# Optimization experiments

Hardware: AMD Instinct MI355X
Metric: run time of the kernel (lower is better)

## Reference

```python
import jax, jax.numpy as jnp
import numpy as np

N, E, H, C, G = 100000, 400000, 4, 64, 64  # nodes, edges, heads, per-head dim, graphs
NEG_SLOPE = 0.2


def gat_conv(x, src, dst, W, a_src, a_dst, b, num_nodes):
    # PyG GATConv (v1), concat=True, eval mode (no dropout).
    h = (x @ W).reshape(num_nodes, H, C)                      # [N,H,C]
    al_src = (h * a_src).sum(-1)                              # [N,H]
    al_dst = (h * a_dst).sum(-1)                              # [N,H]
    e = jax.nn.leaky_relu(al_src[src] + al_dst[dst], NEG_SLOPE)  # [E',H]
    # segment softmax over incoming edges of each destination node
    m = jax.ops.segment_max(e, dst, num_segments=num_nodes)
    m = jnp.where(jnp.isfinite(m), m, 0.0)
    ex = jnp.exp(e - m[dst])
    s = jax.ops.segment_sum(ex, dst, num_segments=num_nodes)
    alpha = ex / (s[dst] + 1e-16)                             # [E',H]
    msg = h[src] * alpha[..., None]                           # [E',H,C]
    out = jax.ops.segment_sum(msg, dst, num_segments=num_nodes)
    return out.reshape(num_nodes, H * C) + b


def setup_inputs() -> dict:
    key = jax.random.key(0)
    ks = jax.random.split(key, 20)
    p = lambda k, shape: (jax.random.normal(k, shape, dtype=jnp.float32) * 0.05)
    inp = {
        "x": jax.random.normal(ks[0], (N, 2), dtype=jnp.float32),
        "edge_index": jax.random.randint(ks[1], (2, E), 0, N, dtype=jnp.int64),
        "batch": jnp.sort(jax.random.randint(ks[2], (N,), 0, G, dtype=jnp.int64)),
        # layer 1: in=2 -> heads*hidden=256
        "W1": p(ks[3], (2, H * C)), "a1s": p(ks[4], (H, C)), "a1d": p(ks[5], (H, C)), "b1": jnp.zeros((H * C,), jnp.float32),
        # layer 2,3: 256 -> 256
        "W2": p(ks[6], (H * C, H * C)), "a2s": p(ks[7], (H, C)), "a2d": p(ks[8], (H, C)), "b2": jnp.zeros((H * C,), jnp.float32),
        "W3": p(ks[9], (H * C, H * C)), "a3s": p(ks[10], (H, C)), "a3d": p(ks[11], (H, C)), "b3": jnp.zeros((H * C,), jnp.float32),
        # projection MLP 256 -> 512 -> 256
        "Wp1": p(ks[12], (H * C, 512)), "bp1": jnp.zeros((512,), jnp.float32),
        "Wp2": p(ks[13], (512, 256)), "bp2": jnp.zeros((256,), jnp.float32),
    }
    return inp


def reference(x, edge_index, batch, W1, a1s, a1d, b1, W2, a2s, a2d, b2,
              W3, a3s, a3d, b3, Wp1, bp1, Wp2, bp2):
    num_nodes = x.shape[0]
    # add_self_loops=True (PyG GATConv default); same edge set for all layers
    loops = jnp.arange(num_nodes, dtype=edge_index.dtype)
    src = jnp.concatenate([edge_index[0], loops])
    dst = jnp.concatenate([edge_index[1], loops])

    h = jax.nn.elu(gat_conv(x, src, dst, W1, a1s, a1d, b1, num_nodes))
    h = jax.nn.elu(gat_conv(h, src, dst, W2, a2s, a2d, b2, num_nodes))
    h = jax.nn.elu(gat_conv(h, src, dst, W3, a3s, a3d, b3, num_nodes))

    # global_mean_pool over graphs
    sums = jax.ops.segment_sum(h, batch, num_segments=G)            # [G,256]
    cnts = jax.ops.segment_sum(jnp.ones((num_nodes,), h.dtype), batch, num_segments=G)
    pooled = sums / jnp.maximum(cnts, 1.0)[:, None]

    # projection MLP (dropout is identity in eval)
    z = jax.nn.relu(pooled @ Wp1 + bp1)
    return z @ Wp2 + bp2
```

## Files before the change

### kernel.cpp

```cpp
#include <hip/hip_runtime.h>
#include <math.h>

#define HC 256
#define NHEAD 4
#define NEG_SLOPE 0.2f
#define GG 64

typedef unsigned short u16;
typedef unsigned int u32;
typedef __attribute__((ext_vector_type(8))) short short8;
typedef __attribute__((ext_vector_type(4))) float f32x4;

static __device__ inline u16 f2bf_rn(float f) {
  u32 x = __float_as_uint(f);
  u32 r = (x + 0x7fffu + ((x >> 16) & 1u)) >> 16;
  return (u16)r;
}
static __device__ inline float bf2f(u16 u) { return __uint_as_float(((u32)u) << 16); }


__global__ void count_deg_kernel(const int* __restrict__ ei, int E, int Nn, int* __restrict__ deg) {
  int idx = blockIdx.x * 256 + threadIdx.x;
  int Et = E + Nn;
  if (idx >= Et) return;
  int d = (idx < E) ? ei[E + idx] : (idx - E);
  atomicAdd(&deg[d], 1);
}

__global__ void scan_partial_kernel(const int* __restrict__ deg, int Nn,
                                    int* __restrict__ rowptr, int* __restrict__ bsum) {
  __shared__ int s[256];
  int t = threadIdx.x, i = blockIdx.x * 256 + t;
  int v = (i < Nn) ? deg[i] : 0;
  s[t] = v; __syncthreads();
  for (int off = 1; off < 256; off <<= 1) {
    int x = (t >= off) ? s[t - off] : 0; __syncthreads();
    s[t] += x; __syncthreads();
  }
  if (i < Nn) rowptr[i] = s[t] - v;
  if (t == 255) bsum[blockIdx.x] = s[t];
}

__global__ void scan_bsum_kernel(int* __restrict__ bsum, int nb) {
  __shared__ int s[512];
  int t = threadIdx.x;
  int v = (t < nb) ? bsum[t] : 0;
  s[t] = v; __syncthreads();
  for (int off = 1; off < 512; off <<= 1) {
    int x = (t >= off) ? s[t - off] : 0; __syncthreads();
    s[t] += x; __syncthreads();
  }
  if (t < nb) bsum[t] = s[t] - v;
}

__global__ void scan_add_kernel(int* __restrict__ rowptr, const int* __restrict__ bsum,
                                int Nn, int Etot) {
  int i = blockIdx.x * 256 + threadIdx.x;
  if (i < Nn) rowptr[i] += bsum[blockIdx.x];
  if (i == 0) rowptr[Nn] = Etot;
}

__global__ void fill_csr_kernel(const int* __restrict__ ei, int E, int Nn,
                                const int* __restrict__ rowptr, int* __restrict__ cursor,
                                int* __restrict__ col) {
  int idx = blockIdx.x * 256 + threadIdx.x;
  int Et = E + Nn;
  if (idx >= Et) return;
  int s, d;
  if (idx < E) { s = ei[idx]; d = ei[E + idx]; } else { s = d = idx - E; }
  int pos = atomicAdd(&cursor[d], 1);
  col[rowptr[d] + pos] = s;
}


__global__ void prep_misc_kernel(const float* __restrict__ W2, const float* __restrict__ W3,
                                 u16* __restrict__ W2t, u16* __restrict__ W3t,
                                 const int* __restrict__ batch, int Nn, int* __restrict__ bounds) {
  int b = blockIdx.x;
  if (b < 512) {
    const float* W = (b < 256) ? W2 : W3;
    u16* dst = (b < 256) ? W2t : W3t;
    int idx = (b & 255) * 256 + threadIdx.x;
    int k = idx >> 8, n = idx & 255;
    dst[n * 256 + k] = f2bf_rn(W[idx]);
  } else {
    int g = threadIdx.x;
    if (g > GG) return;
    int lo = 0, hi = Nn;
    while (lo < hi) { int mid = (lo + hi) >> 1; if (batch[mid] < g) lo = mid + 1; else hi = mid; }
    bounds[g] = lo;
  }
}


__global__ __launch_bounds__(256) void l1_fused_kernel(const float* __restrict__ x,
    const float* __restrict__ W1, const float* __restrict__ a1s, const float* __restrict__ a1d,
    const int* __restrict__ rowptr, const int* __restrict__ col,
    float* __restrict__ xbar, int Nn) {
  __shared__ float va[16];
  int t = threadIdx.x, q = t >> 6, lane = t & 63;
  {
    float asv = a1s[t], adv = a1d[t];
    float w0 = W1[t], w1 = W1[256 + t];
    float s0 = w0 * asv, s1 = w1 * asv, d0 = w0 * adv, d1 = w1 * adv;
    #pragma unroll
    for (int off = 32; off >= 1; off >>= 1) {
      s0 += __shfl_xor(s0, off, 64); s1 += __shfl_xor(s1, off, 64);
      d0 += __shfl_xor(d0, off, 64); d1 += __shfl_xor(d1, off, 64);
    }
    if (lane == 0) { va[q] = s0; va[4 + q] = s1; va[8 + q] = d0; va[12 + q] = d1; }
  }
  __syncthreads();
  int node = blockIdx.x * 256 + t;
  if (node >= Nn) return;
  float4 vs0 = *(const float4*)&va[0], vs1 = *(const float4*)&va[4];
  float4 vd0 = *(const float4*)&va[8], vd1 = *(const float4*)&va[12];
  float2 xv = *(const float2*)&x[(size_t)node * 2];
  float ad0 = xv.x * vd0.x + xv.y * vd1.x;
  float ad1 = xv.x * vd0.y + xv.y * vd1.y;
  float ad2 = xv.x * vd0.z + xv.y * vd1.z;
  float ad3 = xv.x * vd0.w + xv.y * vd1.w;
  int rs = rowptr[node], re = rowptr[node + 1];
  float S0 = 0.f, S1 = 0.f, S2 = 0.f, S3 = 0.f;
  float a0 = 0.f, a1 = 0.f, a2 = 0.f, a3 = 0.f, a4 = 0.f, a5 = 0.f, a6 = 0.f, a7 = 0.f;
  for (int i = rs; i < re; ++i) {
    int s = col[i];
    float2 xs = *(const float2*)&x[(size_t)s * 2];
    float e0 = xs.x * vs0.x + xs.y * vs1.x + ad0; e0 = e0 > 0.f ? e0 : NEG_SLOPE * e0;
    float e1 = xs.x * vs0.y + xs.y * vs1.y + ad1; e1 = e1 > 0.f ? e1 : NEG_SLOPE * e1;
    float e2 = xs.x * vs0.z + xs.y * vs1.z + ad2; e2 = e2 > 0.f ? e2 : NEG_SLOPE * e2;
    float e3 = xs.x * vs0.w + xs.y * vs1.w + ad3; e3 = e3 > 0.f ? e3 : NEG_SLOPE * e3;
    float p0 = __expf(e0), p1 = __expf(e1), p2 = __expf(e2), p3 = __expf(e3);
    S0 += p0; S1 += p1; S2 += p2; S3 += p3;
    a0 += p0 * xs.x; a1 += p0 * xs.y;
    a2 += p1 * xs.x; a3 += p1 * xs.y;
    a4 += p2 * xs.x; a5 += p2 * xs.y;
    a6 += p3 * xs.x; a7 += p3 * xs.y;
  }
  float i0 = 1.f / (S0 + 1e-16f), i1 = 1.f / (S1 + 1e-16f);
  float i2 = 1.f / (S2 + 1e-16f), i3 = 1.f / (S3 + 1e-16f);
  *(float4*)&xbar[(size_t)node * 8]     = make_float4(a0 * i0, a1 * i0, a2 * i1, a3 * i1);
  *(float4*)&xbar[(size_t)node * 8 + 4] = make_float4(a4 * i2, a5 * i2, a6 * i3, a7 * i3);
}

__global__ __launch_bounds__(256) void expand1_kernel(const float* __restrict__ xbar,
    const float* __restrict__ W1, const float* __restrict__ b1,
    u16* __restrict__ out16, int Nn) {
  int node = blockIdx.x * 4 + (threadIdx.x >> 6);
  int lane = threadIdx.x & 63;
  if (node >= Nn) return;
  int hA = lane >> 5;
  float4 xb0 = *(const float4*)&xbar[(size_t)node * 8];
  float4 xb1 = *(const float4*)&xbar[(size_t)node * 8 + 4];
  float xA0 = hA ? xb0.z : xb0.x, xA1 = hA ? xb0.w : xb0.y;
  float xB0 = hA ? xb1.z : xb1.x, xB1 = hA ? xb1.w : xb1.y;
  int cA = 2 * lane, cB = 128 + 2 * lane;
  float2 wA0 = *(const float2*)&W1[cA], wA1 = *(const float2*)&W1[256 + cA];
  float2 wB0 = *(const float2*)&W1[cB], wB1 = *(const float2*)&W1[256 + cB];
  float2 bA = *(const float2*)&b1[cA],  bB = *(const float2*)&b1[cB];
  float o0 = xA0 * wA0.x + xA1 * wA1.x + bA.x;
  float o1 = xA0 * wA0.y + xA1 * wA1.y + bA.y;
  float o2 = xB0 * wB0.x + xB1 * wB1.x + bB.x;
  float o3 = xB0 * wB0.y + xB1 * wB1.y + bB.y;
  o0 = o0 > 0.f ? o0 : (__expf(o0) - 1.0f);
  o1 = o1 > 0.f ? o1 : (__expf(o1) - 1.0f);
  o2 = o2 > 0.f ? o2 : (__expf(o2) - 1.0f);
  o3 = o3 > 0.f ? o3 : (__expf(o3) - 1.0f);
  u32* o32 = (u32*)out16;
  o32[(size_t)node * 128 + lane]      = (u32)f2bf_rn(o0) | ((u32)f2bf_rn(o1) << 16);
  o32[(size_t)node * 128 + 64 + lane] = (u32)f2bf_rn(o2) | ((u32)f2bf_rn(o3) << 16);
}


#define GBM 64
#define GBN 128

__global__ __launch_bounds__(256) void gemm_mfma_kernel(
    const u16* __restrict__ A, const u16* __restrict__ Bt,
    const float* __restrict__ as_, const float* __restrict__ ad_,
    u16* __restrict__ C16, float* __restrict__ als, float* __restrict__ ald, int Mrows) {
  __shared__ __align__(16) u16 smem[24576];
  char* base_ = (char*)smem;
  int bc = blockIdx.x, br = blockIdx.y;
  int tid = threadIdx.x;
  int wid = tid >> 6, lane = tid & 63;
  int wr = wid >> 1, wc = wid & 1;
  int row0 = br * GBM, col0 = bc * GBN;
  int fr = lane & 15, fg = lane >> 4;

  const u16* agp[2];
  int wofA[2];
  #pragma unroll
  for (int p = 0; p < 2; ++p) {
    int row = p * 32 + (tid >> 3), c = tid & 7;
    int gr = row0 + row; if (gr >= Mrows) gr = Mrows - 1;
    agp[p] = A + (size_t)gr * 256 + c * 8;
    wofA[p] = row * 128 + ((c ^ (row & 7)) << 4);
  }
  const u16* bgp[4];
  int wofB[4];
  #pragma unroll
  for (int p = 0; p < 4; ++p) {
    int row = p * 32 + (tid >> 3), c = tid & 7;
    bgp[p] = Bt + (size_t)(col0 + row) * 256 + c * 8;
    wofB[p] = row * 128 + ((c ^ (row & 7)) << 4);
  }
  int rofA[2][2], rofB[2][4];
  #pragma unroll
  for (int ks = 0; ks < 2; ++ks) {
    #pragma unroll
    for (int m = 0; m < 2; ++m) {
      int rl = wr * 32 + m * 16 + fr;
      rofA[ks][m] = rl * 128 + (((ks * 4 + fg) ^ (rl & 7)) << 4);
    }
    #pragma unroll
    for (int n = 0; n < 4; ++n) {
      int cl_ = wc * 64 + n * 16 + fr;
      rofB[ks][n] = cl_ * 128 + (((ks * 4 + fg) ^ (cl_ & 7)) << 4);
    }
  }

  f32x4 acc[2][4];
  #pragma unroll
  for (int m = 0; m < 2; ++m)
    #pragma unroll
    for (int n = 0; n < 4; ++n) acc[m][n] = (f32x4){0.f, 0.f, 0.f, 0.f};

  uint4 va[2], vb[4];
  #pragma unroll
  for (int p = 0; p < 2; ++p) va[p] = *(const uint4*)agp[p];
  #pragma unroll
  for (int p = 0; p < 4; ++p) vb[p] = *(const uint4*)bgp[p];
  #pragma unroll
  for (int p = 0; p < 2; ++p) *(uint4*)(base_ + wofA[p]) = va[p];
  #pragma unroll
  for (int p = 0; p < 4; ++p) *(uint4*)(base_ + 16384 + wofB[p]) = vb[p];
  __syncthreads();

  #pragma unroll
  for (int kt = 0; kt < 4; ++kt) {
    int buf = kt & 1;
    if (kt < 3) {
      #pragma unroll
      for (int p = 0; p < 2; ++p) va[p] = *(const uint4*)(agp[p] + (kt + 1) * 64);
      #pragma unroll
      for (int p = 0; p < 4; ++p) vb[p] = *(const uint4*)(bgp[p] + (kt + 1) * 64);
    }
    #pragma unroll
    for (int ks = 0; ks < 2; ++ks) {
      short8 af[2], bf[4];
      #pragma unroll
      for (int m = 0; m < 2; ++m) af[m] = *(const short8*)(base_ + buf * 8192 + rofA[ks][m]);
      #pragma unroll
      for (int n = 0; n < 4; ++n) bf[n] = *(const short8*)(base_ + 16384 + buf * 16384 + rofB[ks][n]);
      #pragma unroll
      for (int m = 0; m < 2; ++m)
        #pragma unroll
        for (int n = 0; n < 4; ++n)
          acc[m][n] = __builtin_amdgcn_mfma_f32_16x16x32_bf16(af[m], bf[n], acc[m][n], 0, 0, 0);
    }
    if (kt < 3) {
      int nb = buf ^ 1;
      #pragma unroll
      for (int p = 0; p < 2; ++p) *(uint4*)(base_ + nb * 8192 + wofA[p]) = va[p];
      #pragma unroll
      for (int p = 0; p < 4; ++p) *(uint4*)(base_ + 16384 + nb * 16384 + wofB[p]) = vb[p];
      __syncthreads();
    }
  }

  u16* cl = smem;
  __syncthreads();
  #pragma unroll
  for (int m = 0; m < 2; ++m) {
    #pragma unroll
    for (int n = 0; n < 4; ++n) {
      int c = wc * 64 + n * 16 + fr;
      #pragma unroll
      for (int j = 0; j < 4; ++j) {
        int lr = wr * 32 + m * 16 + fg * 4 + j;
        cl[lr * 128 + c] = f2bf_rn(acc[m][n][j]);
      }
    }
  }
  __syncthreads();
  #pragma unroll
  for (int i = 0; i < 4; ++i) {
    int u = i * 256 + tid;
    int lr = u >> 4, ch = u & 15;
    int grow = row0 + lr;
    if (grow < Mrows) {
      uint4 v = *(const uint4*)&cl[lr * 128 + ch * 8];
      *(uint4*)&C16[(size_t)grow * 256 + col0 + ch * 8] = v;
    }
  }

  int head = bc * 2 + wc;
  float asv[4], adv[4];
  #pragma unroll
  for (int n = 0; n < 4; ++n) {
    asv[n] = as_[head * 64 + n * 16 + fr];
    adv[n] = ad_[head * 64 + n * 16 + fr];
  }
  #pragma unroll
  for (int m = 0; m < 2; ++m) {
    #pragma unroll
    for (int j = 0; j < 4; ++j) {
      float ps = 0.f, pd = 0.f;
      #pragma unroll
      for (int n = 0; n < 4; ++n) {
        ps += acc[m][n][j] * asv[n];
        pd += acc[m][n][j] * adv[n];
      }
      #pragma unroll
      for (int off = 1; off < 16; off <<= 1) {
        ps += __shfl_xor(ps, off, 64);
        pd += __shfl_xor(pd, off, 64);
      }
      int grow = row0 + wr * 32 + m * 16 + fg * 4 + j;
      if (fr == 0 && grow < Mrows) {
        als[grow * 4 + head] = ps;
        ald[grow * 4 + head] = pd;
      }
    }
  }
}


__global__ __launch_bounds__(256) void gat_gather_kernel(const u16* __restrict__ h16,
    const float* __restrict__ als, const float* __restrict__ ald,
    const int* __restrict__ rowptr, const int* __restrict__ col,
    const float* __restrict__ bias, u16* __restrict__ out16, int Nn) {
  int node = __builtin_amdgcn_readfirstlane(blockIdx.x * 4 + (threadIdx.x >> 6));
  int lane = threadIdx.x & 63;
  if (node >= Nn) return;
  int rs = rowptr[node], re = rowptr[node + 1];
  int head = lane >> 4;
  float adv = ald[(size_t)node * 4 + head];
  float S = 0.f;
  float a0 = 0.f, a1 = 0.f, a2 = 0.f, a3 = 0.f;
  const uint2* h64 = (const uint2*)h16;
  #pragma unroll 4
  for (int i = rs; i < re; ++i) {
    int s = col[i];
    float e = als[(size_t)s * 4 + head] + adv;
    e = e > 0.f ? e : NEG_SLOPE * e;
    float p = __expf(e);
    S += p;
    uint2 pv = h64[(size_t)s * 64 + lane];
    a0 += p * __uint_as_float(pv.x << 16);
    a1 += p * __uint_as_float(pv.x & 0xffff0000u);
    a2 += p * __uint_as_float(pv.y << 16);
    a3 += p * __uint_as_float(pv.y & 0xffff0000u);
  }
  float iS = 1.f / (S + 1e-16f);
  float4 bv = *(const float4*)&bias[4 * lane];
  float o0 = a0 * iS + bv.x;
  float o1 = a1 * iS + bv.y;
  float o2 = a2 * iS + bv.z;
  float o3 = a3 * iS + bv.w;
  o0 = o0 > 0.f ? o0 : (__expf(o0) - 1.0f);
  o1 = o1 > 0.f ? o1 : (__expf(o1) - 1.0f);
  o2 = o2 > 0.f ? o2 : (__expf(o2) - 1.0f);
  o3 = o3 > 0.f ? o3 : (__expf(o3) - 1.0f);
  uint2 ov;
  ov.x = (u32)f2bf_rn(o0) | ((u32)f2bf_rn(o1) << 16);
  ov.y = (u32)f2bf_rn(o2) | ((u32)f2bf_rn(o3) << 16);
  ((uint2*)out16)[(size_t)node * 64 + lane] = ov;
}


__global__ __launch_bounds__(64) void pool_kernel(const u16* __restrict__ X,
    const int* __restrict__ bounds, float* __restrict__ pooled) {
  int g = blockIdx.x, split = blockIdx.y;
  int lane = threadIdx.x;
  int s = bounds[g], e = bounds[g + 1];
  int cnt = e - s;
  if (cnt <= 0) return;
  int chunk = (cnt + gridDim.y - 1) / gridDim.y;
  int s2 = s + split * chunk, e2 = min(e, s2 + chunk);
  if (s2 >= e2) return;
  int r = lane >> 5, c = lane & 31;
  float acc[8] = {};
  for (int n = s2 + r; n < e2; n += 2) {
    uint4 v = *(const uint4*)&X[(size_t)n * HC + c * 8];
    acc[0] += __uint_as_float(v.x << 16);
    acc[1] += __uint_as_float(v.x & 0xffff0000u);
    acc[2] += __uint_as_float(v.y << 16);
    acc[3] += __uint_as_float(v.y & 0xffff0000u);
    acc[4] += __uint_as_float(v.z << 16);
    acc[5] += __uint_as_float(v.z & 0xffff0000u);
    acc[6] += __uint_as_float(v.w << 16);
    acc[7] += __uint_as_float(v.w & 0xffff0000u);
  }
  #pragma unroll
  for (int j = 0; j < 8; ++j) acc[j] += __shfl_xor(acc[j], 32, 64);
  if (r == 0) {
    #pragma unroll
    for (int j = 0; j < 8; ++j) atomicAdd(&pooled[g * HC + c * 8 + j], acc[j]);
  }
}

__global__ __launch_bounds__(512) void mlp_kernel(const float* __restrict__ pooled,
    const int* __restrict__ bounds, const float* __restrict__ Wp1, const float* __restrict__ bp1,
    const float* __restrict__ Wp2, const float* __restrict__ bp2, float* __restrict__ out) {
  __shared__ float p[256];
  __shared__ float z1[512];
  int g = blockIdx.x, t = threadIdx.x;
  if (t < 256) {
    int cnt = bounds[g + 1] - bounds[g];
    float inv = 1.0f / (float)(cnt > 1 ? cnt : 1);
    p[t] = pooled[g * 256 + t] * inv;
  }
  __syncthreads();
  float a1 = bp1[t];
  for (int k = 0; k < 256; ++k) a1 += p[k] * Wp1[k * 512 + t];
  z1[t] = fmaxf(a1, 0.f);
  __syncthreads();
  if (t < 256) {
    float a2 = bp2[t];
    for (int k = 0; k < 512; ++k) a2 += z1[k] * Wp2[k * 256 + t];
    out[g * 256 + t] = a2;
  }
}


static inline size_t align_up(size_t x, size_t a) { return (x + a - 1) & ~(a - 1); }

extern "C" void kernel_launch(void* const* d_in, const int* in_sizes, int n_in,
                              void* d_out, int out_size, void* d_ws, size_t ws_size,
                              hipStream_t stream) {
  const float* x    = (const float*)d_in[0];
  const int*   ei   = (const int*)d_in[1];
  const int*   batch= (const int*)d_in[2];
  const float* W1   = (const float*)d_in[3];
  const float* a1s  = (const float*)d_in[4];
  const float* a1d  = (const float*)d_in[5];
  const float* b1   = (const float*)d_in[6];
  const float* W2   = (const float*)d_in[7];
  const float* a2s  = (const float*)d_in[8];
  const float* a2d  = (const float*)d_in[9];
  const float* b2   = (const float*)d_in[10];
  const float* W3   = (const float*)d_in[11];
  const float* a3s  = (const float*)d_in[12];
  const float* a3d  = (const float*)d_in[13];
  const float* b3   = (const float*)d_in[14];
  const float* Wp1  = (const float*)d_in[15];
  const float* bp1  = (const float*)d_in[16];
  const float* Wp2  = (const float*)d_in[17];
  const float* bp2  = (const float*)d_in[18];

  const int N = in_sizes[0] / 2;
  const int E = in_sizes[1] / 2;
  const int Et = E + N;

  char* base = (char*)d_ws;
  size_t off = 0;
  auto alloc = [&](size_t bytes) { size_t o = off; off = align_up(off + bytes, 256); return o; };
  u16*   h16    = (u16*)  (base + alloc((size_t)N * HC * 2));
  u16*   xhi    = (u16*)  (base + alloc((size_t)N * HC * 2));
  float* als    = (float*)(base + alloc((size_t)N * 4 * 4));
  float* ald    = (float*)(base + alloc((size_t)N * 4 * 4));
  float* xbar   = (float*)(base + alloc((size_t)N * 8 * 4));
  int*   rowptr = (int*)  (base + alloc((size_t)(N + 1) * 4));
  int*   col    = (int*)  (base + alloc((size_t)Et * 4));
  size_t zoff0 = off;
  int*   deg    = (int*)  (base + alloc((size_t)N * 4));
  int*   cursor = (int*)  (base + alloc((size_t)N * 4));
  float* pooled = (float*)(base + alloc((size_t)GG * HC * 4));
  size_t zbytes = off - zoff0;
  int*   bsum   = (int*)  (base + alloc(512 * 4));
  int*   bounds = (int*)  (base + alloc((GG + 1) * 4));
  (void)ws_size; (void)n_in; (void)out_size;

  u16* W2t = (u16*)deg;
  u16* W3t = (u16*)cursor;

  hipMemsetAsync(base + zoff0, 0, zbytes, stream);

  int ebk = (Et + 255) / 256;
  count_deg_kernel<<<ebk, 256, 0, stream>>>(ei, E, N, deg);
  int NT = (N + 255) / 256;
  scan_partial_kernel<<<NT, 256, 0, stream>>>(deg, N, rowptr, bsum);
  scan_bsum_kernel<<<1, 512, 0, stream>>>(bsum, NT);
  scan_add_kernel<<<NT, 256, 0, stream>>>(rowptr, bsum, N, Et);
  fill_csr_kernel<<<ebk, 256, 0, stream>>>(ei, E, N, rowptr, cursor, col);

  prep_misc_kernel<<<513, 256, 0, stream>>>(W2, W3, W2t, W3t, batch, N, bounds);

  dim3 gemm_grid(HC / GBN, (N + GBM - 1) / GBM);
  int nodeblk = (N + 3) / 4;

  l1_fused_kernel<<<NT, 256, 0, stream>>>(x, W1, a1s, a1d, rowptr, col, xbar, N);
  expand1_kernel<<<nodeblk, 256, 0, stream>>>(xbar, W1, b1, xhi, N);
  gemm_mfma_kernel<<<gemm_grid, 256, 0, stream>>>(xhi, W2t, a2s, a2d, h16, als, ald, N);
  gat_gather_kernel<<<nodeblk, 256, 0, stream>>>(h16, als, ald, rowptr, col, b2, xhi, N);
  gemm_mfma_kernel<<<gemm_grid, 256, 0, stream>>>(xhi, W3t, a3s, a3d, h16, als, ald, N);
  gat_gather_kernel<<<nodeblk, 256, 0, stream>>>(h16, als, ald, rowptr, col, b3, xhi, N);

  pool_kernel<<<dim3(GG, 32), 64, 0, stream>>>(xhi, bounds, pooled);
  mlp_kernel<<<GG, 512, 0, stream>>>(pooled, bounds, Wp1, bp1, Wp2, bp2, (float*)d_out);
}
```

Before: 321.7 us.

## Fuse layer-1 expand into aggregation kernel and shrink GEMM row tile

The layer-1 aggregation kernel now keeps its per-node 8-float aggregates in shared memory and expands them through W1, bias and ELU to bf16 output in the same kernel. This removes the separate expand kernel launch and the xbar global round trip. Separately, the MFMA GEMM row tile drops from 64 to 32, so each wave computes one 16-row fragment. That doubles the number of GEMM blocks and lowers per-block registers and LDS, but B-tile reuse per block is halved.

```diff
diff --git a/kernel.cpp b/kernel.cpp
--- a/kernel.cpp
+++ b/kernel.cpp
@@ -95,10 +95,11 @@
 
 __global__ __launch_bounds__(256) void l1_fused_kernel(const float* __restrict__ x,
     const float* __restrict__ W1, const float* __restrict__ a1s, const float* __restrict__ a1d,
-    const int* __restrict__ rowptr, const int* __restrict__ col,
-    float* __restrict__ xbar, int Nn) {
+    const float* __restrict__ b1, const int* __restrict__ rowptr, const int* __restrict__ col,
+    u16* __restrict__ out16, int Nn) {
   __shared__ float va[16];
-  int t = threadIdx.x, q = t >> 6, lane = t & 63;
+  __shared__ float xb_s[256][8];
+  int t = threadIdx.x, q = t >> 6, lane = t & 63, wid = t >> 6;
   {
     float asv = a1s[t], adv = a1d[t];
     float w0 = W1[t], w1 = W1[256 + t];
@@ -111,75 +112,78 @@
     if (lane == 0) { va[q] = s0; va[4 + q] = s1; va[8 + q] = d0; va[12 + q] = d1; }
   }
   __syncthreads();
-  int node = blockIdx.x * 256 + t;
-  if (node >= Nn) return;
-  float4 vs0 = *(const float4*)&va[0], vs1 = *(const float4*)&va[4];
-  float4 vd0 = *(const float4*)&va[8], vd1 = *(const float4*)&va[12];
-  float2 xv = *(const float2*)&x[(size_t)node * 2];
-  float ad0 = xv.x * vd0.x + xv.y * vd1.x;
-  float ad1 = xv.x * vd0.y + xv.y * vd1.y;
-  float ad2 = xv.x * vd0.z + xv.y * vd1.z;
-  float ad3 = xv.x * vd0.w + xv.y * vd1.w;
-  int rs = rowptr[node], re = rowptr[node + 1];
-  float S0 = 0.f, S1 = 0.f, S2 = 0.f, S3 = 0.f;
-  float a0 = 0.f, a1 = 0.f, a2 = 0.f, a3 = 0.f, a4 = 0.f, a5 = 0.f, a6 = 0.f, a7 = 0.f;
-  for (int i = rs; i < re; ++i) {
-    int s = col[i];
-    float2 xs = *(const float2*)&x[(size_t)s * 2];
-    float e0 = xs.x * vs0.x + xs.y * vs1.x + ad0; e0 = e0 > 0.f ? e0 : NEG_SLOPE * e0;
-    float e1 = xs.x * vs0.y + xs.y * vs1.y + ad1; e1 = e1 > 0.f ? e1 : NEG_SLOPE * e1;
-    float e2 = xs.x * vs0.z + xs.y * vs1.z + ad2; e2 = e2 > 0.f ? e2 : NEG_SLOPE * e2;
-    float e3 = xs.x * vs0.w + xs.y * vs1.w + ad3; e3 = e3 > 0.f ? e3 : NEG_SLOPE * e3;
-    float p0 = __expf(e0), p1 = __expf(e1), p2 = __expf(e2), p3 = __expf(e3);
-    S0 += p0; S1 += p1; S2 += p2; S3 += p3;
-    a0 += p0 * xs.x; a1 += p0 * xs.y;
-    a2 += p1 * xs.x; a3 += p1 * xs.y;
-    a4 += p2 * xs.x; a5 += p2 * xs.y;
-    a6 += p3 * xs.x; a7 += p3 * xs.y;
-  }
-  float i0 = 1.f / (S0 + 1e-16f), i1 = 1.f / (S1 + 1e-16f);
-  float i2 = 1.f / (S2 + 1e-16f), i3 = 1.f / (S3 + 1e-16f);
-  *(float4*)&xbar[(size_t)node * 8]     = make_float4(a0 * i0, a1 * i0, a2 * i1, a3 * i1);
-  *(float4*)&xbar[(size_t)node * 8 + 4] = make_float4(a4 * i2, a5 * i2, a6 * i3, a7 * i3);
-}
-
-__global__ __launch_bounds__(256) void expand1_kernel(const float* __restrict__ xbar,
-    const float* __restrict__ W1, const float* __restrict__ b1,
-    u16* __restrict__ out16, int Nn) {
-  int node = blockIdx.x * 4 + (threadIdx.x >> 6);
-  int lane = threadIdx.x & 63;
-  if (node >= Nn) return;
+  int base = blockIdx.x * 256;
+  int node = base + t;
+  if (node < Nn) {
+    float4 vs0 = *(const float4*)&va[0], vs1 = *(const float4*)&va[4];
+    float4 vd0 = *(const float4*)&va[8], vd1 = *(const float4*)&va[12];
+    float2 xv = *(const float2*)&x[(size_t)node * 2];
+    float ad0 = xv.x * vd0.x + xv.y * vd1.x;
+    float ad1 = xv.x * vd0.y + xv.y * vd1.y;
+    float ad2 = xv.x * vd0.z + xv.y * vd1.z;
+    float ad3 = xv.x * vd0.w + xv.y * vd1.w;
+    int rs = rowptr[node], re = rowptr[node + 1];
+    float S0 = 0.f, S1 = 0.f, S2 = 0.f, S3 = 0.f;
+    float a0 = 0.f, a1 = 0.f, a2 = 0.f, a3 = 0.f, a4 = 0.f, a5 = 0.f, a6 = 0.f, a7 = 0.f;
+    for (int i = rs; i < re; ++i) {
+      int s = col[i];
+      float2 xs = *(const float2*)&x[(size_t)s * 2];
+      float e0 = xs.x * vs0.x + xs.y * vs1.x + ad0; e0 = e0 > 0.f ? e0 : NEG_SLOPE * e0;
+      float e1 = xs.x * vs0.y + xs.y * vs1.y + ad1; e1 = e1 > 0.f ? e1 : NEG_SLOPE * e1;
+      float e2 = xs.x * vs0.z + xs.y * vs1.z + ad2; e2 = e2 > 0.f ? e2 : NEG_SLOPE * e2;
+      float e3 = xs.x * vs0.w + xs.y * vs1.w + ad3; e3 = e3 > 0.f ? e3 : NEG_SLOPE * e3;
+      float p0 = __expf(e0), p1 = __expf(e1), p2 = __expf(e2), p3 = __expf(e3);
+      S0 += p0; S1 += p1; S2 += p2; S3 += p3;
+      a0 += p0 * xs.x; a1 += p0 * xs.y;
+      a2 += p1 * xs.x; a3 += p1 * xs.y;
+      a4 += p2 * xs.x; a5 += p2 * xs.y;
+      a6 += p3 * xs.x; a7 += p3 * xs.y;
+    }
+    float i0 = 1.f / (S0 + 1e-16f), i1 = 1.f / (S1 + 1e-16f);
+    float i2 = 1.f / (S2 + 1e-16f), i3 = 1.f / (S3 + 1e-16f);
+    xb_s[t][0] = a0 * i0; xb_s[t][1] = a1 * i0;
+    xb_s[t][2] = a2 * i1; xb_s[t][3] = a3 * i1;
+    xb_s[t][4] = a4 * i2; xb_s[t][5] = a5 * i2;
+    xb_s[t][6] = a6 * i3; xb_s[t][7] = a7 * i3;
+  }
+  __syncthreads();
   int hA = lane >> 5;
-  float4 xb0 = *(const float4*)&xbar[(size_t)node * 8];
-  float4 xb1 = *(const float4*)&xbar[(size_t)node * 8 + 4];
-  float xA0 = hA ? xb0.z : xb0.x, xA1 = hA ? xb0.w : xb0.y;
-  float xB0 = hA ? xb1.z : xb1.x, xB1 = hA ? xb1.w : xb1.y;
   int cA = 2 * lane, cB = 128 + 2 * lane;
   float2 wA0 = *(const float2*)&W1[cA], wA1 = *(const float2*)&W1[256 + cA];
   float2 wB0 = *(const float2*)&W1[cB], wB1 = *(const float2*)&W1[256 + cB];
   float2 bA = *(const float2*)&b1[cA],  bB = *(const float2*)&b1[cB];
-  float o0 = xA0 * wA0.x + xA1 * wA1.x + bA.x;
-  float o1 = xA0 * wA0.y + xA1 * wA1.y + bA.y;
-  float o2 = xB0 * wB0.x + xB1 * wB1.x + bB.x;
-  float o3 = xB0 * wB0.y + xB1 * wB1.y + bB.y;
-  o0 = o0 > 0.f ? o0 : (__expf(o0) - 1.0f);
-  o1 = o1 > 0.f ? o1 : (__expf(o1) - 1.0f);
-  o2 = o2 > 0.f ? o2 : (__expf(o2) - 1.0f);
-  o3 = o3 > 0.f ? o3 : (__expf(o3) - 1.0f);
   u32* o32 = (u32*)out16;
-  o32[(size_t)node * 128 + lane]      = (u32)f2bf_rn(o0) | ((u32)f2bf_rn(o1) << 16);
-  o32[(size_t)node * 128 + 64 + lane] = (u32)f2bf_rn(o2) | ((u32)f2bf_rn(o3) << 16);
-}
-
-
-#define GBM 64
+  #pragma unroll 4
+  for (int it = 0; it < 64; ++it) {
+    int slot = it * 4 + wid;
+    int nd = base + slot;
+    if (nd >= Nn) break;
+    float xA0 = hA ? xb_s[slot][2] : xb_s[slot][0];
+    float xA1 = hA ? xb_s[slot][3] : xb_s[slot][1];
+    float xB0 = hA ? xb_s[slot][6] : xb_s[slot][4];
+    float xB1 = hA ? xb_s[slot][7] : xb_s[slot][5];
+    float o0 = xA0 * wA0.x + xA1 * wA1.x + bA.x;
+    float o1 = xA0 * wA0.y + xA1 * wA1.y + bA.y;
+    float o2 = xB0 * wB0.x + xB1 * wB1.x + bB.x;
+    float o3 = xB0 * wB0.y + xB1 * wB1.y + bB.y;
+    o0 = o0 > 0.f ? o0 : (__expf(o0) - 1.0f);
+    o1 = o1 > 0.f ? o1 : (__expf(o1) - 1.0f);
+    o2 = o2 > 0.f ? o2 : (__expf(o2) - 1.0f);
+    o3 = o3 > 0.f ? o3 : (__expf(o3) - 1.0f);
+    o32[(size_t)nd * 128 + lane]      = (u32)f2bf_rn(o0) | ((u32)f2bf_rn(o1) << 16);
+    o32[(size_t)nd * 128 + 64 + lane] = (u32)f2bf_rn(o2) | ((u32)f2bf_rn(o3) << 16);
+  }
+}
+
+
+#define GBM 32
 #define GBN 128
 
 __global__ __launch_bounds__(256) void gemm_mfma_kernel(
     const u16* __restrict__ A, const u16* __restrict__ Bt,
     const float* __restrict__ as_, const float* __restrict__ ad_,
     u16* __restrict__ C16, float* __restrict__ als, float* __restrict__ ald, int Mrows) {
-  __shared__ __align__(16) u16 smem[24576];
+  __shared__ __align__(16) u16 smem[20480];
   char* base_ = (char*)smem;
   int bc = blockIdx.x, br = blockIdx.y;
   int tid = threadIdx.x;
@@ -188,14 +192,13 @@
   int row0 = br * GBM, col0 = bc * GBN;
   int fr = lane & 15, fg = lane >> 4;
 
-  const u16* agp[2];
-  int wofA[2];
-  #pragma unroll
-  for (int p = 0; p < 2; ++p) {
-    int row = p * 32 + (tid >> 3), c = tid & 7;
+  const u16* agp;
+  int wofA;
+  {
+    int row = tid >> 3, c = tid & 7;
     int gr = row0 + row; if (gr >= Mrows) gr = Mrows - 1;
-    agp[p] = A + (size_t)gr * 256 + c * 8;
-    wofA[p] = row * 128 + ((c ^ (row & 7)) << 4);
+    agp = A + (size_t)gr * 256 + c * 8;
+    wofA = row * 128 + ((c ^ (row & 7)) << 4);
   }
   const u16* bgp[4];
   int wofB[4];
@@ -205,14 +208,11 @@
     bgp[p] = Bt + (size_t)(col0 + row) * 256 + c * 8;
     wofB[p] = row * 128 + ((c ^ (row & 7)) << 4);
   }
-  int rofA[2][2], rofB[2][4];
+  int rofA[2], rofB[2][4];
   #pragma unroll
   for (int ks = 0; ks < 2; ++ks) {
-    #pragma unroll
-    for (int m = 0; m < 2; ++m) {
-      int rl = wr * 32 + m * 16 + fr;
-      rofA[ks][m] = rl * 128 + (((ks * 4 + fg) ^ (rl & 7)) << 4);
-    }
+    int rl = wr * 16 + fr;
+    rofA[ks] = rl * 128 + (((ks * 4 + fg) ^ (rl & 7)) << 4);
     #pragma unroll
     for (int n = 0; n < 4; ++n) {
       int cl_ = wc * 64 + n * 16 + fr;
@@ -220,51 +220,42 @@
     }
   }
 
-  f32x4 acc[2][4];
-  #pragma unroll
-  for (int m = 0; m < 2; ++m)
-    #pragma unroll
-    for (int n = 0; n < 4; ++n) acc[m][n] = (f32x4){0.f, 0.f, 0.f, 0.f};
-
-  uint4 va[2], vb[4];
-  #pragma unroll
-  for (int p = 0; p < 2; ++p) va[p] = *(const uint4*)agp[p];
+  f32x4 acc[4];
+  #pragma unroll
+  for (int n = 0; n < 4; ++n) acc[n] = (f32x4){0.f, 0.f, 0.f, 0.f};
+
+  uint4 va, vb[4];
+  va = *(const uint4*)agp;
   #pragma unroll
   for (int p = 0; p < 4; ++p) vb[p] = *(const uint4*)bgp[p];
-  #pragma unroll
-  for (int p = 0; p < 2; ++p) *(uint4*)(base_ + wofA[p]) = va[p];
-  #pragma unroll
-  for (int p = 0; p < 4; ++p) *(uint4*)(base_ + 16384 + wofB[p]) = vb[p];
+  *(uint4*)(base_ + wofA) = va;
+  #pragma unroll
+  for (int p = 0; p < 4; ++p) *(uint4*)(base_ + 8192 + wofB[p]) = vb[p];
   __syncthreads();
 
   #pragma unroll
   for (int kt = 0; kt < 4; ++kt) {
     int buf = kt & 1;
     if (kt < 3) {
-      #pragma unroll
-      for (int p = 0; p < 2; ++p) va[p] = *(const uint4*)(agp[p] + (kt + 1) * 64);
+      va = *(const uint4*)(agp + (kt + 1) * 64);
       #pragma unroll
       for (int p = 0; p < 4; ++p) vb[p] = *(const uint4*)(bgp[p] + (kt + 1) * 64);
     }
     #pragma unroll
     for (int ks = 0; ks < 2; ++ks) {
-      short8 af[2], bf[4];
+      short8 af = *(const short8*)(base_ + buf * 4096 + rofA[ks]);
+      short8 bf[4];
       #pragma unroll
-      for (int m = 0; m < 2; ++m) af[m] = *(const short8*)(base_ + buf * 8192 + rofA[ks][m]);
+      for (int n = 0; n < 4; ++n) bf[n] = *(const short8*)(base_ + 8192 + buf * 16384 + rofB[ks][n]);
       #pragma unroll
-      for (int n = 0; n < 4; ++n) bf[n] = *(const short8*)(base_ + 16384 + buf * 16384 + rofB[ks][n]);
-      #pragma unroll
-      for (int m = 0; m < 2; ++m)
-        #pragma unroll
-        for (int n = 0; n < 4; ++n)
-          acc[m][n] = __builtin_amdgcn_mfma_f32_16x16x32_bf16(af[m], bf[n], acc[m][n], 0, 0, 0);
+      for (int n = 0; n < 4; ++n)
+        acc[n] = __builtin_amdgcn_mfma_f32_16x16x32_bf16(af, bf[n], acc[n], 0, 0, 0);
     }
     if (kt < 3) {
       int nb = buf ^ 1;
+      *(uint4*)(base_ + nb * 4096 + wofA) = va;
       #pragma unroll
-      for (int p = 0; p < 2; ++p) *(uint4*)(base_ + nb * 8192 + wofA[p]) = va[p];
-      #pragma unroll
-      for (int p = 0; p < 4; ++p) *(uint4*)(base_ + 16384 + nb * 16384 + wofB[p]) = vb[p];
+      for (int p = 0; p < 4; ++p) *(uint4*)(base_ + 8192 + nb * 16384 + wofB[p]) = vb[p];
       __syncthreads();
     }
   }
@@ -272,20 +263,17 @@
   u16* cl = smem;
   __syncthreads();
   #pragma unroll
-  for (int m = 0; m < 2; ++m) {
-    #pragma unroll
-    for (int n = 0; n < 4; ++n) {
-      int c = wc * 64 + n * 16 + fr;
-      #pragma unroll
-      for (int j = 0; j < 4; ++j) {
-        int lr = wr * 32 + m * 16 + fg * 4 + j;
-        cl[lr * 128 + c] = f2bf_rn(acc[m][n][j]);
-      }
-    }
-  }
-  __syncthreads();
-  #pragma unroll
-  for (int i = 0; i < 4; ++i) {
+  for (int n = 0; n < 4; ++n) {
+    int c = wc * 64 + n * 16 + fr;
+    #pragma unroll
+    for (int j = 0; j < 4; ++j) {
+      int lr = wr * 16 + fg * 4 + j;
+      cl[lr * 128 + c] = f2bf_rn(acc[n][j]);
+    }
+  }
+  __syncthreads();
+  #pragma unroll
+  for (int i = 0; i < 2; ++i) {
     int u = i * 256 + tid;
     int lr = u >> 4, ch = u & 15;
     int grow = row0 + lr;
@@ -303,25 +291,22 @@
     adv[n] = ad_[head * 64 + n * 16 + fr];
   }
   #pragma unroll
-  for (int m = 0; m < 2; ++m) {
-    #pragma unroll
-    for (int j = 0; j < 4; ++j) {
-      float ps = 0.f, pd = 0.f;
-      #pragma unroll
-      for (int n = 0; n < 4; ++n) {
-        ps += acc[m][n][j] * asv[n];
-        pd += acc[m][n][j] * adv[n];
-      }
-      #pragma unroll
-      for (int off = 1; off < 16; off <<= 1) {
-        ps += __shfl_xor(ps, off, 64);
-        pd += __shfl_xor(pd, off, 64);
-      }
-      int grow = row0 + wr * 32 + m * 16 + fg * 4 + j;
-      if (fr == 0 && grow < Mrows) {
-        als[grow * 4 + head] = ps;
-        ald[grow * 4 + head] = pd;
-      }
+  for (int j = 0; j < 4; ++j) {
+    float ps = 0.f, pd = 0.f;
+    #pragma unroll
+    for (int n = 0; n < 4; ++n) {
+      ps += acc[n][j] * asv[n];
+      pd += acc[n][j] * adv[n];
+    }
+    #pragma unroll
+    for (int off = 1; off < 16; off <<= 1) {
+      ps += __shfl_xor(ps, off, 64);
+      pd += __shfl_xor(pd, off, 64);
+    }
+    int grow = row0 + wr * 16 + fg * 4 + j;
+    if (fr == 0 && grow < Mrows) {
+      als[grow * 4 + head] = ps;
+      ald[grow * 4 + head] = pd;
     }
   }
 }
@@ -461,7 +446,6 @@
   u16*   xhi    = (u16*)  (base + alloc((size_t)N * HC * 2));
   float* als    = (float*)(base + alloc((size_t)N * 4 * 4));
   float* ald    = (float*)(base + alloc((size_t)N * 4 * 4));
-  float* xbar   = (float*)(base + alloc((size_t)N * 8 * 4));
   int*   rowptr = (int*)  (base + alloc((size_t)(N + 1) * 4));
   int*   col    = (int*)  (base + alloc((size_t)Et * 4));
   size_t zoff0 = off;
@@ -491,8 +475,7 @@
   dim3 gemm_grid(HC / GBN, (N + GBM - 1) / GBM);
   int nodeblk = (N + 3) / 4;
 
-  l1_fused_kernel<<<NT, 256, 0, stream>>>(x, W1, a1s, a1d, rowptr, col, xbar, N);
-  expand1_kernel<<<nodeblk, 256, 0, stream>>>(xbar, W1, b1, xhi, N);
+  l1_fused_kernel<<<NT, 256, 0, stream>>>(x, W1, a1s, a1d, b1, rowptr, col, xhi, N);
   gemm_mfma_kernel<<<gemm_grid, 256, 0, stream>>>(xhi, W2t, a2s, a2d, h16, als, ald, N);
   gat_gather_kernel<<<nodeblk, 256, 0, stream>>>(h16, als, ald, rowptr, col, b2, xhi, N);
   gemm_mfma_kernel<<<gemm_grid, 256, 0, stream>>>(xhi, W3t, a3s, a3d, h16, als, ald, N);
```

Measured after the change: 319.4 us (median of 2 runs). About the same (-0.7%).
